# Optimization experiments

Measured on AMD Instinct MI355X. Metric: run time of the kernel, lower is better.

## Reference

```python
import jax, jax.numpy as jnp
import numpy as np

B, S, D = 2, 2048, 1024
H = 16
DH = D // H  # 64


def setup_inputs() -> dict:
    key = jax.random.key(0)
    k1, k2, k3 = jax.random.split(key, 3)
    x = jax.random.normal(k1, (B, S, D), dtype=jnp.float32)
    W_qkv = jax.random.normal(k2, (D, 3 * D), dtype=jnp.float32) * 0.01
    b_qkv = jnp.zeros((3 * D,), dtype=jnp.float32)
    W_out = jax.random.normal(k3, (D, D), dtype=jnp.float32) * 0.01
    b_out = jnp.zeros((D,), dtype=jnp.float32)
    return {"x": x, "W_qkv": W_qkv, "b_qkv": b_qkv, "W_out": W_out, "b_out": b_out}


def reference(x, W_qkv, b_qkv, W_out, b_out):
    b, s, d = x.shape
    h, dh = H, DH
    # fused QKV projection
    qkv = x @ W_qkv + b_qkv                       # [b, s, 3d]
    qkv = qkv.reshape(b, s, 3, h, dh)
    q, k, v = qkv[:, :, 0], qkv[:, :, 1], qkv[:, :, 2]  # [b, s, h, dh]
    q = q.transpose(0, 2, 1, 3)                    # [b, h, s, dh]
    k = k.transpose(0, 2, 1, 3)
    v = v.transpose(0, 2, 1, 3)
    inv_sqrt_d = jnp.asarray(1.0 / np.sqrt(dh), dtype=x.dtype)
    scores = jnp.einsum('bhqd,bhkd->bhqk', q, k) * inv_sqrt_d  # [b, h, s, s]
    causal = jnp.tril(jnp.ones((s, s), dtype=bool))[None, None]
    # source masks with -10000.0 (not -inf)
    scores = jnp.where(causal, scores, jnp.asarray(-10000.0, dtype=scores.dtype))
    probs = jax.nn.softmax(scores, axis=-1)
    attn = jnp.einsum('bhqk,bhkd->bhqd', probs, v)  # [b, h, s, dh]
    attn = attn.transpose(0, 2, 1, 3).reshape(b, s, d)
    return attn @ W_out + b_out
```

## Files before the change

### kernel.cpp

```cpp
#include <hip/hip_runtime.h>
#include <hip/hip_bf16.h>

#define B_  2
#define S_  2048
#define D_  1024
#define H_  16
#define DH_ 64
#define M_  (B_ * S_)
#define QKV_LD (3 * D_)

typedef __bf16 bf16x8 __attribute__((ext_vector_type(8)));
typedef float  f32x4  __attribute__((ext_vector_type(4)));
typedef unsigned short us4 __attribute__((ext_vector_type(4)));
typedef unsigned short us8 __attribute__((ext_vector_type(8)));

__device__ inline unsigned short f2bf(float f) {
  union { __bf16 h; unsigned short u; } cv; cv.h = (__bf16)f; return cv.u;
}
__device__ inline float bf2f(unsigned short u) {
  union { unsigned int i; float f; } cv; cv.i = ((unsigned int)u) << 16; return cv.f;
}
__device__ inline unsigned int pk2bf(float lo, float hi) {
  return (unsigned int)f2bf(lo) | ((unsigned int)f2bf(hi) << 16);
}
__device__ inline void cstore(float* p, float v) { *p = v; }
__device__ inline void cstore(unsigned short* p, float v) { *p = f2bf(v); }

__device__ inline void gload_lds16(const void* g, void* lds) {
  __builtin_amdgcn_global_load_lds(
      (const __attribute__((address_space(1))) unsigned int*)g,
      (__attribute__((address_space(3))) unsigned int*)lds, 16, 0, 0);
}

__global__ __launch_bounds__(256) void prep_all(
    const float* __restrict__ x, unsigned short* __restrict__ x_bf,
    const float* __restrict__ W_qkv, unsigned short* __restrict__ wqkvT,
    const float* __restrict__ W_out, unsigned short* __restrict__ woutT) {
  __shared__ float tile[32][33];
  const int blk = blockIdx.x;
  const int t = threadIdx.x;
  if (blk < 4096) {
    int i = blk * 256 + t;
    float4 v = ((const float4*)x)[i];
    us4 p = { f2bf(v.x), f2bf(v.y), f2bf(v.z), f2bf(v.w) };
    ((us4*)x_bf)[i] = p;
    return;
  }
  const float* W; unsigned short* Wt; int K, N, bi;
  if (blk < 4096 + 3072) { bi = blk - 4096; W = W_qkv; Wt = wqkvT; K = D_; N = QKV_LD; }
  else                   { bi = blk - 7168; W = W_out; Wt = woutT; K = D_; N = D_; }
  const int bx = bi % (N / 32), by = bi / (N / 32);
  const int tx = t & 31, ty = t >> 5;
  const int c0 = bx * 32, r0 = by * 32;
  #pragma unroll
  for (int i = 0; i < 4; ++i)
    tile[ty + 8 * i][tx] = W[(size_t)(r0 + ty + 8 * i) * N + c0 + tx];
  __syncthreads();
  #pragma unroll
  for (int i = 0; i < 4; ++i)
    Wt[(size_t)(c0 + ty + 8 * i) * K + r0 + tx] = f2bf(tile[tx][ty + 8 * i]);
}

template<typename CT>
__global__ __launch_bounds__(256) void gemm_bf16_tn(
    const unsigned short* __restrict__ A,
    const unsigned short* __restrict__ Bt,
    const float* __restrict__ bias,
    CT* __restrict__ C, int N, int K) {
  __shared__ __align__(16) unsigned short smA[128 * 32];
  __shared__ __align__(16) unsigned short smB[128 * 32];
  const int t = threadIdx.x;
  const int w = t >> 6, l = t & 63;
  const int lg = l >> 4, lr = l & 15;
  const int row0 = blockIdx.y * 128, col0 = blockIdx.x * 128;
  const int wm = (w >> 1) * 64, wn = (w & 1) * 64;

  f32x4 acc[4][4] = {};

  for (int k0 = 0; k0 < K; k0 += 32) {
    __syncthreads();
    #pragma unroll
    for (int i = 0; i < 2; ++i) {
      const int inst = 2 * w + i;
      const int r = inst * 16 + (l >> 2);
      const int cb = (l & 3) * 8;
      gload_lds16(A  + (size_t)(row0 + r) * K + k0 + cb, &smA[inst * 512]);
      gload_lds16(Bt + (size_t)(col0 + r) * K + k0 + cb, &smB[inst * 512]);
    }
    __syncthreads();

    bf16x8 af[4], bfr[4];
    #pragma unroll
    for (int m = 0; m < 4; ++m)
      af[m] = *(const bf16x8*)&smA[(wm + m * 16 + lr) * 32 + lg * 8];
    #pragma unroll
    for (int n = 0; n < 4; ++n)
      bfr[n] = *(const bf16x8*)&smB[(wn + n * 16 + lr) * 32 + lg * 8];
    #pragma unroll
    for (int m = 0; m < 4; ++m)
      #pragma unroll
      for (int n = 0; n < 4; ++n)
        acc[m][n] = __builtin_amdgcn_mfma_f32_16x16x32_bf16(af[m], bfr[n], acc[m][n], 0, 0, 0);
  }

  #pragma unroll
  for (int m = 0; m < 4; ++m) {
    #pragma unroll
    for (int n = 0; n < 4; ++n) {
      const int col = col0 + wn + n * 16 + lr;
      const float bv = bias[col];
      #pragma unroll
      for (int r = 0; r < 4; ++r) {
        const int row = row0 + wm + m * 16 + lg * 4 + r;
        cstore(&C[(size_t)row * N + col], acc[m][n][r] + bv);
      }
    }
  }
}

__global__ __launch_bounds__(256) void attn_fwd_mfma(
    const unsigned short* __restrict__ qkv, unsigned short* __restrict__ attn_out) {
  const int bid = blockIdx.x + gridDim.x * blockIdx.y;
  const int xcd = bid & 7;
  const int li  = bid >> 3;
  const int bh  = xcd * 4 + (li >> 4);
  const int x   = li & 15;
  const int b = bh / H_, h = bh % H_;
  const unsigned short* base = qkv + (size_t)b * S_ * QKV_LD;

  __shared__ __align__(16) char smK[2][64 * 128];
  __shared__ __align__(16) char smV[2][64 * 128];

  const int t  = threadIdx.x;
  const int w  = t >> 6;
  const int l  = t & 63;
  const int lg = l >> 4;
  const int lr = l & 15;

  const unsigned short* kbase = base + D_ + h * DH_;
  const unsigned short* vbase = base + 2 * D_ + h * DH_;

  us8 kreg[2], vreg[2];
  const int kp  = (t & 31) * 2;
  const int vdb = (t >> 5) * 8;

  auto issue_loads = [&](int k0) {
    #pragma unroll
    for (int it = 0; it < 2; ++it) {
      int idx = t + it * 256;
      int r = idx >> 3, c = idx & 7;
      kreg[it] = *(const us8*)(kbase + (size_t)(k0 + r) * QKV_LD + c * 8);
    }
    vreg[0] = *(const us8*)(vbase + (size_t)(k0 + kp) * QKV_LD + vdb);
    vreg[1] = *(const us8*)(vbase + (size_t)(k0 + kp + 1) * QKV_LD + vdb);
  };
  auto write_lds = [&](int buf) {
    #pragma unroll
    for (int it = 0; it < 2; ++it) {
      int idx = t + it * 256;
      int r = idx >> 3, c = idx & 7;
      int rho = (r & 0x23) | ((r & 0x04) << 2) | ((r & 0x18) >> 1);
      *(us8*)(smK[buf] + rho * 128 + ((c * 16) ^ ((rho & 7) << 4))) = kreg[it];
    }
    #pragma unroll
    for (int j = 0; j < 8; ++j) {
      int row = vdb + j;
      unsigned int pv = (unsigned int)vreg[0][j] | ((unsigned int)vreg[1][j] << 16);
      *(unsigned int*)(smV[buf] + row * 128 + ((2 * kp) ^ ((row & 7) << 4))) = pv;
    }
  };

  #pragma unroll 1
  for (int sel = 0; sel < 2; ++sel) {
    const int qt = sel ? (31 - x) : x;
    const int q0 = qt * 64;
    const int qw0 = q0 + w * 16;

    bf16x8 qf[2];
    {
      const unsigned short* qp = base + (size_t)(qw0 + lr) * QKV_LD + h * DH_ + 8 * lg;
      #pragma unroll
      for (int ks = 0; ks < 2; ++ks) {
        us8 qv = *(const us8*)(qp + 32 * ks);
        #pragma unroll
        for (int e = 0; e < 8; ++e) qf[ks][e] = (__bf16)(bf2f(qv[e]) * 0.18033688f);
      }
    }

    float mrun = -1e30f, lrun = 0.f;
    f32x4 acc_o[4] = {};

    const int ntiles = qt + 1;
    issue_loads(0);
    write_lds(0);
    __syncthreads();

    for (int kti = 0; kti < ntiles; ++kti) {
      const int k0 = kti * 64;
      const int cur = kti & 1;

      if (kti + 1 < ntiles) issue_loads((kti + 1) * 64);

      if (k0 <= qw0 + 15) {
        f32x4 sc[4] = {};
        #pragma unroll
        for (int kt = 0; kt < 4; ++kt)
          #pragma unroll
          for (int ks = 0; ks < 2; ++ks) {
            int row = kt * 16 + lr;
            bf16x8 kb_ = *(const bf16x8*)(smK[cur] + row * 128 +
                                          (((ks * 64) + 16 * lg) ^ ((row & 7) << 4)));
            sc[kt] = __builtin_amdgcn_mfma_f32_16x16x32_bf16(kb_, qf[ks], sc[kt], 0, 0, 0);
          }

        if (k0 + 63 > qw0) {
          #pragma unroll
          for (int kt = 0; kt < 4; ++kt)
            #pragma unroll
            for (int r = 0; r < 4; ++r) {
              int kc = k0 + ((kt >> 1) << 5) + (lg << 3) + ((kt & 1) << 2) + r;
              if (kc > qw0 + lr) sc[kt][r] = -1e30f;
            }
        }

        float v = fmaxf(fmaxf(sc[0][0], sc[0][1]), fmaxf(sc[0][2], sc[0][3]));
        #pragma unroll
        for (int kt = 1; kt < 4; ++kt)
          v = fmaxf(v, fmaxf(fmaxf(sc[kt][0], sc[kt][1]), fmaxf(sc[kt][2], sc[kt][3])));
        v = fmaxf(v, __shfl_xor(v, 16));
        v = fmaxf(v, __shfl_xor(v, 32));
        if (!__all(v <= mrun + 8.0f)) {
          const float mnew = fmaxf(mrun, v);
          const float alpha = exp2f(mrun - mnew);
          mrun = mnew;
          float alphaO[4];
          #pragma unroll
          for (int r = 0; r < 4; ++r)
            alphaO[r] = __shfl(alpha, (l & 48) | (lg * 4 + r));
          #pragma unroll
          for (int dt = 0; dt < 4; ++dt)
            #pragma unroll
            for (int r = 0; r < 4; ++r) acc_o[dt][r] *= alphaO[r];
          lrun *= alpha;
        }
        float s = 0.f;
        #pragma unroll
        for (int kt = 0; kt < 4; ++kt)
          #pragma unroll
          for (int r = 0; r < 4; ++r) {
            float p = exp2f(sc[kt][r] - mrun);
            sc[kt][r] = p;
            s += p;
          }
        s += __shfl_xor(s, 16);
        s += __shfl_xor(s, 32);
        lrun += s;

        union { unsigned int u[4]; bf16x8 v8; } pa[2];
        #pragma unroll
        for (int ks = 0; ks < 2; ++ks) {
          pa[ks].u[0] = pk2bf(sc[2 * ks][0], sc[2 * ks][1]);
          pa[ks].u[1] = pk2bf(sc[2 * ks][2], sc[2 * ks][3]);
          pa[ks].u[2] = pk2bf(sc[2 * ks + 1][0], sc[2 * ks + 1][1]);
          pa[ks].u[3] = pk2bf(sc[2 * ks + 1][2], sc[2 * ks + 1][3]);
        }

        #pragma unroll
        for (int dt = 0; dt < 4; ++dt)
          #pragma unroll
          for (int ks = 0; ks < 2; ++ks) {
            int row = dt * 16 + lr;
            bf16x8 vb = *(const bf16x8*)(smV[cur] + row * 128 +
                                         (((ks * 64) + 16 * lg) ^ ((row & 7) << 4)));
            acc_o[dt] = __builtin_amdgcn_mfma_f32_16x16x32_bf16(pa[ks].v8, vb, acc_o[dt], 0, 0, 0);
          }
      }

      if (kti + 1 < ntiles) write_lds(cur ^ 1);
      __syncthreads();
    }

    const float inv = 1.0f / lrun;
    float invO[4];
    #pragma unroll
    for (int r = 0; r < 4; ++r)
      invO[r] = __shfl(inv, (l & 48) | (lg * 4 + r));
    #pragma unroll
    for (int dt = 0; dt < 4; ++dt)
      #pragma unroll
      for (int r = 0; r < 4; ++r)
        attn_out[(size_t)(b * S_ + qw0 + lg * 4 + r) * D_ + h * DH_ + dt * 16 + lr] =
            f2bf(acc_o[dt][r] * invO[r]);
  }
}

extern "C" void kernel_launch(void* const* d_in, const int* in_sizes, int n_in,
                              void* d_out, int out_size, void* d_ws, size_t ws_size,
                              hipStream_t stream) {
  const float* x     = (const float*)d_in[0];
  const float* W_qkv = (const float*)d_in[1];
  const float* b_qkv = (const float*)d_in[2];
  const float* W_out = (const float*)d_in[3];
  const float* b_out = (const float*)d_in[4];
  float* out = (float*)d_out;

  char* ws = (char*)d_ws;
  unsigned short* qkv_bf  = (unsigned short*)ws;  ws += (size_t)M_ * QKV_LD * 2;
  unsigned short* attn_bf = (unsigned short*)ws;  ws += (size_t)M_ * D_ * 2;
  unsigned short* x_bf    = (unsigned short*)ws;  ws += (size_t)M_ * D_ * 2;
  unsigned short* wqkvT   = (unsigned short*)ws;  ws += (size_t)QKV_LD * D_ * 2;
  unsigned short* woutT   = (unsigned short*)ws;

  dim3 blk(256);
  prep_all<<<4096 + 3072 + 1024, blk, 0, stream>>>(x, x_bf, W_qkv, wqkvT, W_out, woutT);
  gemm_bf16_tn<unsigned short><<<dim3(QKV_LD / 128, M_ / 128), blk, 0, stream>>>(
      x_bf, wqkvT, b_qkv, qkv_bf, QKV_LD, D_);
  attn_fwd_mfma<<<dim3(S_ / 64 / 2, B_ * H_), blk, 0, stream>>>(qkv_bf, attn_bf);
  gemm_bf16_tn<float><<<dim3(D_ / 128, M_ / 128), blk, 0, stream>>>(
      attn_bf, woutT, b_out, out, D_, D_);
}
```

Measured before the change: 127.7 us.

## Process paired causal query tiles concurrently in one 512-thread attention block

Each attention block previously handled two query tiles (x and 31-x) one after the other with 256 threads. Now it runs 8 waves: four handle the short tile and four the long tile, sharing a single pass of K/V tiles loaded into LDS. This avoids reloading K/V for the short tile and removes the serial second pass. In exchange the short-tile waves sit idle once their causal range ends, and the larger block with launch_bounds(512,4) limits registers per thread.

Result: faster. 121.8 us (-4.6%).

```diff
diff --git a/kernel.cpp b/kernel.cpp
--- a/kernel.cpp
+++ b/kernel.cpp
@@ -118,9 +118,9 @@
   }
 }
 
-__global__ __launch_bounds__(256) void attn_fwd_mfma(
+__global__ __launch_bounds__(512, 4) void attn_fwd_mfma(
     const unsigned short* __restrict__ qkv, unsigned short* __restrict__ attn_out) {
-  const int bid = blockIdx.x + gridDim.x * blockIdx.y;
+  const int bid = blockIdx.x;
   const int xcd = bid & 7;
   const int li  = bid >> 3;
   const int bh  = xcd * 4 + (li >> 4);
@@ -133,16 +133,21 @@
 
   const int t  = threadIdx.x;
   const int w  = t >> 6;
+  const bool lo = (w < 4);
+  const int wq = w & 3;
   const int l  = t & 63;
   const int lg = l >> 4;
   const int lr = l & 15;
 
+  const int qt  = lo ? x : (31 - x);
+  const int qw0 = qt * 64 + wq * 16;
+
   const unsigned short* kbase = base + D_ + h * DH_;
   const unsigned short* vbase = base + 2 * D_ + h * DH_;
 
   us8 kreg[2], vreg[2];
   const int kp  = (t & 31) * 2;
-  const int vdb = (t >> 5) * 8;
+  const int vdb = ((t >> 5) & 7) * 8;
 
   auto issue_loads = [&](int k0) {
     #pragma unroll
@@ -170,128 +175,121 @@
     }
   };
 
-  #pragma unroll 1
-  for (int sel = 0; sel < 2; ++sel) {
-    const int qt = sel ? (31 - x) : x;
-    const int q0 = qt * 64;
-    const int qw0 = q0 + w * 16;
-
-    bf16x8 qf[2];
-    {
-      const unsigned short* qp = base + (size_t)(qw0 + lr) * QKV_LD + h * DH_ + 8 * lg;
-      #pragma unroll
-      for (int ks = 0; ks < 2; ++ks) {
-        us8 qv = *(const us8*)(qp + 32 * ks);
-        #pragma unroll
-        for (int e = 0; e < 8; ++e) qf[ks][e] = (__bf16)(bf2f(qv[e]) * 0.18033688f);
-      }
-    }
-
-    float mrun = -1e30f, lrun = 0.f;
-    f32x4 acc_o[4] = {};
-
-    const int ntiles = qt + 1;
-    issue_loads(0);
-    write_lds(0);
-    __syncthreads();
-
-    for (int kti = 0; kti < ntiles; ++kti) {
-      const int k0 = kti * 64;
-      const int cur = kti & 1;
-
-      if (kti + 1 < ntiles) issue_loads((kti + 1) * 64);
-
-      if (k0 <= qw0 + 15) {
-        f32x4 sc[4] = {};
-        #pragma unroll
-        for (int kt = 0; kt < 4; ++kt)
-          #pragma unroll
-          for (int ks = 0; ks < 2; ++ks) {
-            int row = kt * 16 + lr;
-            bf16x8 kb_ = *(const bf16x8*)(smK[cur] + row * 128 +
-                                          (((ks * 64) + 16 * lg) ^ ((row & 7) << 4)));
-            sc[kt] = __builtin_amdgcn_mfma_f32_16x16x32_bf16(kb_, qf[ks], sc[kt], 0, 0, 0);
-          }
-
-        if (k0 + 63 > qw0) {
-          #pragma unroll
-          for (int kt = 0; kt < 4; ++kt)
-            #pragma unroll
-            for (int r = 0; r < 4; ++r) {
-              int kc = k0 + ((kt >> 1) << 5) + (lg << 3) + ((kt & 1) << 2) + r;
-              if (kc > qw0 + lr) sc[kt][r] = -1e30f;
-            }
+  bf16x8 qf[2];
+  {
+    const unsigned short* qp = base + (size_t)(qw0 + lr) * QKV_LD + h * DH_ + 8 * lg;
+    #pragma unroll
+    for (int ks = 0; ks < 2; ++ks) {
+      us8 qv = *(const us8*)(qp + 32 * ks);
+      #pragma unroll
+      for (int e = 0; e < 8; ++e) qf[ks][e] = (__bf16)(bf2f(qv[e]) * 0.18033688f);
+    }
+  }
+
+  float mrun = -1e30f, lrun = 0.f;
+  f32x4 acc_o[4] = {};
+
+  const int ntiles = 32 - x;
+  if (t < 256) { issue_loads(0); write_lds(0); }
+  __syncthreads();
+
+  for (int kti = 0; kti < ntiles; ++kti) {
+    const int k0 = kti * 64;
+    const int cur = kti & 1;
+
+    if (t < 256 && kti + 1 < ntiles) issue_loads((kti + 1) * 64);
+
+    const bool active = lo ? (kti <= x) : true;
+    if (active) {
+      f32x4 sc[4] = {};
+      #pragma unroll
+      for (int kt = 0; kt < 4; ++kt)
+        #pragma unroll
+        for (int ks = 0; ks < 2; ++ks) {
+          int row = kt * 16 + lr;
+          bf16x8 kb_ = *(const bf16x8*)(smK[cur] + row * 128 +
+                                        (((ks * 64) + 16 * lg) ^ ((row & 7) << 4)));
+          sc[kt] = __builtin_amdgcn_mfma_f32_16x16x32_bf16(kb_, qf[ks], sc[kt], 0, 0, 0);
         }
 
-        float v = fmaxf(fmaxf(sc[0][0], sc[0][1]), fmaxf(sc[0][2], sc[0][3]));
-        #pragma unroll
-        for (int kt = 1; kt < 4; ++kt)
-          v = fmaxf(v, fmaxf(fmaxf(sc[kt][0], sc[kt][1]), fmaxf(sc[kt][2], sc[kt][3])));
-        v = fmaxf(v, __shfl_xor(v, 16));
-        v = fmaxf(v, __shfl_xor(v, 32));
-        if (!__all(v <= mrun + 8.0f)) {
-          const float mnew = fmaxf(mrun, v);
-          const float alpha = exp2f(mrun - mnew);
-          mrun = mnew;
-          float alphaO[4];
-          #pragma unroll
-          for (int r = 0; r < 4; ++r)
-            alphaO[r] = __shfl(alpha, (l & 48) | (lg * 4 + r));
-          #pragma unroll
-          for (int dt = 0; dt < 4; ++dt)
-            #pragma unroll
-            for (int r = 0; r < 4; ++r) acc_o[dt][r] *= alphaO[r];
-          lrun *= alpha;
-        }
-        float s = 0.f;
+      if (k0 + 63 > qw0) {
         #pragma unroll
         for (int kt = 0; kt < 4; ++kt)
           #pragma unroll
           for (int r = 0; r < 4; ++r) {
-            float p = exp2f(sc[kt][r] - mrun);
-            sc[kt][r] = p;
-            s += p;
+            int kc = k0 + ((kt >> 1) << 5) + (lg << 3) + ((kt & 1) << 2) + r;
+            if (kc > qw0 + lr) sc[kt][r] = -1e30f;
           }
-        s += __shfl_xor(s, 16);
-        s += __shfl_xor(s, 32);
-        lrun += s;
-
-        union { unsigned int u[4]; bf16x8 v8; } pa[2];
-        #pragma unroll
-        for (int ks = 0; ks < 2; ++ks) {
-          pa[ks].u[0] = pk2bf(sc[2 * ks][0], sc[2 * ks][1]);
-          pa[ks].u[1] = pk2bf(sc[2 * ks][2], sc[2 * ks][3]);
-          pa[ks].u[2] = pk2bf(sc[2 * ks + 1][0], sc[2 * ks + 1][1]);
-          pa[ks].u[3] = pk2bf(sc[2 * ks + 1][2], sc[2 * ks + 1][3]);
-        }
-
+      }
+
+      float v = fmaxf(fmaxf(sc[0][0], sc[0][1]), fmaxf(sc[0][2], sc[0][3]));
+      #pragma unroll
+      for (int kt = 1; kt < 4; ++kt)
+        v = fmaxf(v, fmaxf(fmaxf(sc[kt][0], sc[kt][1]), fmaxf(sc[kt][2], sc[kt][3])));
+      v = fmaxf(v, __shfl_xor(v, 16));
+      v = fmaxf(v, __shfl_xor(v, 32));
+      if (!__all(v <= mrun + 8.0f)) {
+        const float mnew = fmaxf(mrun, v);
+        const float alpha = exp2f(mrun - mnew);
+        mrun = mnew;
+        float alphaO[4];
+        #pragma unroll
+        for (int r = 0; r < 4; ++r)
+          alphaO[r] = __shfl(alpha, (l & 48) | (lg * 4 + r));
         #pragma unroll
         for (int dt = 0; dt < 4; ++dt)
           #pragma unroll
-          for (int ks = 0; ks < 2; ++ks) {
-            int row = dt * 16 + lr;
-            bf16x8 vb = *(const bf16x8*)(smV[cur] + row * 128 +
-                                         (((ks * 64) + 16 * lg) ^ ((row & 7) << 4)));
-            acc_o[dt] = __builtin_amdgcn_mfma_f32_16x16x32_bf16(pa[ks].v8, vb, acc_o[dt], 0, 0, 0);
-          }
+          for (int r = 0; r < 4; ++r) acc_o[dt][r] *= alphaO[r];
+        lrun *= alpha;
       }
-
-      if (kti + 1 < ntiles) write_lds(cur ^ 1);
-      __syncthreads();
-    }
-
-    const float inv = 1.0f / lrun;
-    float invO[4];
+      float s = 0.f;
+      #pragma unroll
+      for (int kt = 0; kt < 4; ++kt)
+        #pragma unroll
+        for (int r = 0; r < 4; ++r) {
+          float p = exp2f(sc[kt][r] - mrun);
+          sc[kt][r] = p;
+          s += p;
+        }
+      s += __shfl_xor(s, 16);
+      s += __shfl_xor(s, 32);
+      lrun += s;
+
+      union { unsigned int u[4]; bf16x8 v8; } pa[2];
+      #pragma unroll
+      for (int ks = 0; ks < 2; ++ks) {
+        pa[ks].u[0] = pk2bf(sc[2 * ks][0], sc[2 * ks][1]);
+        pa[ks].u[1] = pk2bf(sc[2 * ks][2], sc[2 * ks][3]);
+        pa[ks].u[2] = pk2bf(sc[2 * ks + 1][0], sc[2 * ks + 1][1]);
+        pa[ks].u[3] = pk2bf(sc[2 * ks + 1][2], sc[2 * ks + 1][3]);
+      }
+
+      #pragma unroll
+      for (int dt = 0; dt < 4; ++dt)
+        #pragma unroll
+        for (int ks = 0; ks < 2; ++ks) {
+          int row = dt * 16 + lr;
+          bf16x8 vb = *(const bf16x8*)(smV[cur] + row * 128 +
+                                       (((ks * 64) + 16 * lg) ^ ((row & 7) << 4)));
+          acc_o[dt] = __builtin_amdgcn_mfma_f32_16x16x32_bf16(pa[ks].v8, vb, acc_o[dt], 0, 0, 0);
+        }
+    }
+
+    if (t < 256 && kti + 1 < ntiles) write_lds(cur ^ 1);
+    __syncthreads();
+  }
+
+  const float inv = 1.0f / lrun;
+  float invO[4];
+  #pragma unroll
+  for (int r = 0; r < 4; ++r)
+    invO[r] = __shfl(inv, (l & 48) | (lg * 4 + r));
+  #pragma unroll
+  for (int dt = 0; dt < 4; ++dt)
     #pragma unroll
     for (int r = 0; r < 4; ++r)
-      invO[r] = __shfl(inv, (l & 48) | (lg * 4 + r));
-    #pragma unroll
-    for (int dt = 0; dt < 4; ++dt)
-      #pragma unroll
-      for (int r = 0; r < 4; ++r)
-        attn_out[(size_t)(b * S_ + qw0 + lg * 4 + r) * D_ + h * DH_ + dt * 16 + lr] =
-            f2bf(acc_o[dt][r] * invO[r]);
-  }
+      attn_out[(size_t)(b * S_ + qw0 + lg * 4 + r) * D_ + h * DH_ + dt * 16 + lr] =
+          f2bf(acc_o[dt][r] * invO[r]);
 }
 
 extern "C" void kernel_launch(void* const* d_in, const int* in_sizes, int n_in,
@@ -315,7 +313,7 @@
   prep_all<<<4096 + 3072 + 1024, blk, 0, stream>>>(x, x_bf, W_qkv, wqkvT, W_out, woutT);
   gemm_bf16_tn<unsigned short><<<dim3(QKV_LD / 128, M_ / 128), blk, 0, stream>>>(
       x_bf, wqkvT, b_qkv, qkv_bf, QKV_LD, D_);
-  attn_fwd_mfma<<<dim3(S_ / 64 / 2, B_ * H_), blk, 0, stream>>>(qkv_bf, attn_bf);
+  attn_fwd_mfma<<<dim3(512), dim3(512), 0, stream>>>(qkv_bf, attn_bf);
   gemm_bf16_tn<float><<<dim3(D_ / 128, M_ / 128), blk, 0, stream>>>(
       attn_bf, woutT, b_out, out, D_, D_);
 }
```
